# Performance work log

Hardware: AMD Instinct MI355X
Metric: run time of the kernel (lower is better)

The kernel has to match this reference:

```python
import jax, jax.numpy as jnp
import numpy as np

B, T, C, H, D = 2, 2048, 768, 12, 64
ATTN_MULT = 0.125  # 1/sqrt(head_dim)


def setup_inputs() -> dict:
    key = jax.random.key(0)
    k0, k1, k2 = jax.random.split(key, 3)
    x = jax.random.normal(k0, (B, T, C), jnp.float32)
    w_attn = jax.random.normal(k1, (3 * H * D, C), jnp.float32) * 0.02
    b_attn = jnp.zeros((3 * H * D,), jnp.float32)
    w_proj = jax.random.normal(k2, (C, H * D), jnp.float32) * 0.02
    b_proj = jnp.zeros((C,), jnp.float32)
    return {"x": x, "w_attn": w_attn, "b_attn": b_attn, "w_proj": w_proj, "b_proj": b_proj}


def reference(x, w_attn, b_attn, w_proj, b_proj):
    Bx, Tx, Cx = x.shape
    # fused qkv projection (torch nn.Linear: x @ W^T + b)
    qkv = x @ w_attn.T + b_attn                      # [B,T,3*H*D]
    q, k, v = jnp.split(qkv, 3, axis=2)
    def to_heads(t):
        return t.reshape(Bx, Tx, H, D).transpose(0, 2, 1, 3)  # [B,H,T,D]
    q, k, v = to_heads(q), to_heads(k), to_heads(v)
    att = jnp.einsum('bhqd,bhkd->bhqk', q, k) * ATTN_MULT     # [B,H,T,T]

    causal = jnp.tril(jnp.ones((Tx, Tx), dtype=bool))
    # selection scores from head 0 (selective attention)
    S = jax.nn.relu(att[:, 0])                                # [B,T,T]
    # prevent_from_masking_myself: zero diagonal; protect_bos_token: zero key col 0
    smask = causal & ~jnp.eye(Tx, dtype=bool)
    smask = smask.at[:, 0].set(False)
    S = jnp.where(smask, S, 0.0)
    # exclusive cumulative sum over the query dim: F[i,j] = sum_{i'<i} S[i',j]
    Fmask = jnp.cumsum(S, axis=-2) - S                        # [B,T,T]
    att = att - Fmask[:, None]                                # broadcast over heads

    att = jnp.where(causal, att, -jnp.inf)
    p = jax.nn.softmax(att, axis=-1)                          # [B,H,T,T]
    y = jnp.einsum('bhqk,bhkd->bhqd', p, v)                   # [B,H,T,D]
    y = y.transpose(0, 2, 1, 3).reshape(Bx, Tx, H * D)
    return y @ w_proj.T + b_proj
```

## Files before the change

kernel.cpp:

```cpp
#include <hip/hip_runtime.h>
#include <hip/hip_bf16.h>

#define BB 2
#define TT 2048
#define CC 768
#define HH 12
#define DD 64
#define NQKV 2304
#define MTOT (BB*TT)
#define CH 32
#define NCH (TT/CH)

typedef __bf16 bf16x8 __attribute__((ext_vector_type(8)));
typedef __bf16 bf16x4 __attribute__((ext_vector_type(4)));
typedef float  f32x4  __attribute__((ext_vector_type(4)));

__device__ __forceinline__ f32x4 mfma16(bf16x8 a, bf16x8 b, f32x4 c) {
    return __builtin_amdgcn_mfma_f32_16x16x32_bf16(a, b, c, 0, 0, 0);
}

__device__ __forceinline__ void load_lds16(const void* g, void* l) {
    __builtin_amdgcn_global_load_lds(
        (const __attribute__((address_space(1))) void*)g,
        (__attribute__((address_space(3))) void*)l, 16, 0, 0);
}

__global__ __launch_bounds__(256) void cvt_bf16_kernel(
    const float* __restrict__ x, const float* __restrict__ wa, const float* __restrict__ wp,
    __bf16* __restrict__ xb, __bf16* __restrict__ wab, __bf16* __restrict__ wpb)
{
    const long NX = (long)MTOT * CC;
    const long NWA = (long)NQKV * CC;
    long idx = ((long)blockIdx.x * 256 + threadIdx.x) * 4;
    const float* src; __bf16* dst; long off;
    if (idx < NX)            { src = x;  dst = xb;  off = idx; }
    else if (idx < NX + NWA) { src = wa; dst = wab; off = idx - NX; }
    else                     { src = wp; dst = wpb; off = idx - NX - NWA; }
    float4 v = *(const float4*)(src + off);
    bf16x4 o;
    o[0] = (__bf16)v.x; o[1] = (__bf16)v.y; o[2] = (__bf16)v.z; o[3] = (__bf16)v.w;
    *(bf16x4*)(dst + off) = o;
}

template<int EPI>
__global__ __launch_bounds__(256, 2) void gemm_nt_kernel(
    const __bf16* __restrict__ A, const __bf16* __restrict__ Bw,
    const float* __restrict__ bias,
    __bf16* __restrict__ oQ, __bf16* __restrict__ oK, __bf16* __restrict__ oVT,
    float* __restrict__ oOut, int K)
{
    __shared__ __align__(16) __bf16 As[128 * 32];
    __shared__ __align__(16) __bf16 Bs[128 * 32];
    const int tid = threadIdx.x;
    const int m0 = blockIdx.y * 128, n0 = blockIdx.x * 128;
    const int w = tid >> 6, lane = tid & 63, quad = lane >> 4, l16 = lane & 15;
    const int wm = (w >> 1) * 64, wn = (w & 1) * 64;
    const int grow = w * 16 + (lane >> 2);
    const int gcol = (lane & 3) * 8;
    __bf16* AsW = As + w * 512;
    __bf16* BsW = Bs + w * 512;

    f32x4 acc[4][4] = {};

    for (int kt = 0; kt < K; kt += 32) {
        __syncthreads();
        load_lds16(A  + (long)(m0 + grow) * K + kt + gcol,      AsW);
        load_lds16(A  + (long)(m0 + grow + 64) * K + kt + gcol, AsW + 2048);
        load_lds16(Bw + (long)(n0 + grow) * K + kt + gcol,      BsW);
        load_lds16(Bw + (long)(n0 + grow + 64) * K + kt + gcol, BsW + 2048);
        __syncthreads();

        bf16x8 af[4], bfr[4];
#pragma unroll
        for (int g = 0; g < 4; g++)  af[g]  = *(const bf16x8*)(As + (wm + g * 16 + l16) * 32 + quad * 8);
#pragma unroll
        for (int jb = 0; jb < 4; jb++) bfr[jb] = *(const bf16x8*)(Bs + (wn + jb * 16 + l16) * 32 + quad * 8);
#pragma unroll
        for (int g = 0; g < 4; g++)
#pragma unroll
            for (int jb = 0; jb < 4; jb++)
                acc[g][jb] = mfma16(af[g], bfr[jb], acc[g][jb]);
    }

#pragma unroll
    for (int jb = 0; jb < 4; jb++) {
        const int n = n0 + wn + jb * 16 + l16;
        const float bv = bias[n];
#pragma unroll
        for (int g = 0; g < 4; g++) {
#pragma unroll
            for (int r = 0; r < 4; r++) {
                const int m = m0 + wm + g * 16 + quad * 4 + r;
                const float v = acc[g][jb][r] + bv;
                if (EPI == 0) {
                    const int which = n / 768;
                    const int rem = n - which * 768;
                    const int h = rem >> 6, d = rem & 63;
                    const int b = m >> 11, t = m & 2047;
                    const __bf16 hv = (__bf16)v;
                    if (which == 0)      oQ [(((b * HH + h) * TT + t) << 6) + d] = hv;
                    else if (which == 1) oK [(((b * HH + h) * TT + t) << 6) + d] = hv;
                    else                 oVT[((((b * HH + h) << 6) + d) * TT) + t] = hv;
                } else {
                    oOut[(long)m * CC + n] = v;
                }
            }
        }
    }
}

__global__ __launch_bounds__(256) void sgemm_kernel(
    const __bf16* __restrict__ q, const __bf16* __restrict__ k, float* __restrict__ S)
{
    const int tj = blockIdx.x, ti = blockIdx.y, b = blockIdx.z;
    if (tj > ti) return;
    const int w = threadIdx.x >> 6, lane = threadIdx.x & 63, quad = lane >> 4, l16 = lane & 15;
    const int i0 = ti * 64 + w * 16;

    const __bf16* qp = q + (((long)(b * HH + 0) * TT + i0 + l16) << 6) + quad * 8;
    bf16x8 a0 = *(const bf16x8*)qp, a1 = *(const bf16x8*)(qp + 32);
    const __bf16* kbase = k + ((long)(b * HH + 0) * TT << 6);

#pragma unroll
    for (int jb = 0; jb < 4; jb++) {
        const __bf16* kp = kbase + (((long)(tj * 64 + jb * 16 + l16)) << 6) + quad * 8;
        bf16x8 b0 = *(const bf16x8*)kp, b1 = *(const bf16x8*)(kp + 32);
        f32x4 acc = {};
        acc = mfma16(a0, b0, acc);
        acc = mfma16(a1, b1, acc);
        const int j = tj * 64 + jb * 16 + l16;
#pragma unroll
        for (int r = 0; r < 4; r++) {
            const int i = i0 + quad * 4 + r;
            float v = fmaxf(acc[r] * 0.125f, 0.0f);
            v = (j >= 1 && j < i) ? v : 0.0f;
            S[((long)b * TT + i) * TT + j] = v;
        }
    }
}

__global__ __launch_bounds__(256) void scan_sum_kernel(
    const float* __restrict__ S, float* __restrict__ csum)
{
    const int j = blockIdx.x * 256 + threadIdx.x;
    const int chunk = blockIdx.y, b = blockIdx.z;
    const int ib = chunk * CH;
    const float* p = S + ((long)b * TT + ib) * TT + j;
    float s = 0.0f;
#pragma unroll
    for (int ii = 0; ii < CH; ii++) {
        float v = p[(long)ii * TT];
        s += ((ib + ii) > j) ? v : 0.0f;
    }
    csum[(b * NCH + chunk) * TT + j] = s;
}

__global__ __launch_bounds__(256) void scan_prefix_kernel(float* __restrict__ csum)
{
    const int idx = blockIdx.x * 256 + threadIdx.x;
    const int b = idx >> 11, j = idx & 2047;
    float vals[NCH];
#pragma unroll
    for (int c = 0; c < NCH; c++) vals[c] = csum[(b * NCH + c) * TT + j];
    float off = 0.0f;
#pragma unroll
    for (int c = 0; c < NCH; c++) { float t = vals[c]; vals[c] = off; off += t; }
#pragma unroll
    for (int c = 0; c < NCH; c++) csum[(b * NCH + c) * TT + j] = vals[c];
}

__global__ __launch_bounds__(256) void scan_write_kernel(
    float* __restrict__ S, const float* __restrict__ csum)
{
    const int j = blockIdx.x * 256 + threadIdx.x;
    const int chunk = blockIdx.y, b = blockIdx.z;
    const int ib = chunk * CH;
    float off = csum[(b * NCH + chunk) * TT + j];
    float* p = S + ((long)b * TT + ib) * TT + j;
#pragma unroll
    for (int ii = 0; ii < CH; ii++) {
        float v = p[(long)ii * TT];
        v = ((ib + ii) > j) ? v : 0.0f;
        p[(long)ii * TT] = off;
        off += v;
    }
}

__global__ __launch_bounds__(256, 3) void flash_kernel(
    const __bf16* __restrict__ q, const __bf16* __restrict__ k, const __bf16* __restrict__ vT,
    const float* __restrict__ F, __bf16* __restrict__ y)
{
    __shared__ __align__(16) __bf16 Ks[64 * 64];
    __shared__ __align__(16) __bf16 Vs[64 * 64];
    __shared__ __align__(16) __bf16 Pls[4][16 * 72];
    const int qt = 31 - blockIdx.x;
    const int h = blockIdx.y, b = blockIdx.z;
    const int w = threadIdx.x >> 6, lane = threadIdx.x & 63, quad = lane >> 4, l16 = lane & 15;
    const int i0 = qt * 64 + w * 16;

    const __bf16* qp = q + (((long)(b * HH + h) * TT + i0 + l16) << 6) + quad * 8;
    const bf16x8 aq0 = *(const bf16x8*)qp;
    const bf16x8 aq1 = *(const bf16x8*)(qp + 32);
    const __bf16* kb = k  + ((long)(b * HH + h) * TT << 6);
    const __bf16* vb = vT + ((long)(b * HH + h) * TT << 6);
    const float*  Fb = F  + (long)b * TT * TT + (long)i0 * TT;
    __bf16* Pl = &Pls[w][0];

    const int rl = lane >> 3;
    const int cs8 = ((lane & 7) ^ rl) * 8;
    __bf16* KsW = Ks + w * 1024;
    __bf16* VsW = Vs + w * 1024;
    const int sw0 = ((quad)     ^ (l16 & 7)) * 8;
    const int sw1 = ((quad + 4) ^ (l16 & 7)) * 8;

    f32x4 O[4] = {};
    float lr[4] = {0.0f, 0.0f, 0.0f, 0.0f};

    float Fn[4][4];
#pragma unroll
    for (int jh = 0; jh < 4; jh++)
#pragma unroll
        for (int r = 0; r < 4; r++)
            Fn[jh][r] = Fb[(long)(quad * 4 + r) * TT + jh * 16 + l16];

    const int jtend = qt * 64;
    for (int jt = 0; jt <= jtend; jt += 64) {
        __syncthreads();
        load_lds16(kb + ((long)(jt + w * 16 + rl) << 6) + cs8,     KsW);
        load_lds16(kb + ((long)(jt + w * 16 + 8 + rl) << 6) + cs8, KsW + 512);
        load_lds16(vb + (long)(w * 16 + rl) * TT + jt + cs8,       VsW);
        load_lds16(vb + (long)(w * 16 + 8 + rl) * TT + jt + cs8,   VsW + 512);
        float Fc[4][4];
#pragma unroll
        for (int jh = 0; jh < 4; jh++)
#pragma unroll
            for (int r = 0; r < 4; r++)
                Fc[jh][r] = Fn[jh][r];
        const int jn = (jt + 64 <= jtend) ? jt + 64 : jt;
#pragma unroll
        for (int jh = 0; jh < 4; jh++)
#pragma unroll
            for (int r = 0; r < 4; r++)
                Fn[jh][r] = Fb[(long)(quad * 4 + r) * TT + jn + jh * 16 + l16];
        __builtin_amdgcn_sched_barrier(0);
        __syncthreads();
        float sc[4][4];
#pragma unroll
        for (int jh = 0; jh < 4; jh++) {
            const bf16x8 kc0 = *(const bf16x8*)(Ks + ((jh * 16 + l16) << 6) + sw0);
            const bf16x8 kc1 = *(const bf16x8*)(Ks + ((jh * 16 + l16) << 6) + sw1);
            f32x4 acc = {};
            acc = mfma16(aq0, kc0, acc);
            acc = mfma16(aq1, kc1, acc);
#pragma unroll
            for (int r = 0; r < 4; r++) sc[jh][r] = acc[r];
        }
        const bool masked = (jt + 63 > i0);
#pragma unroll
        for (int jh = 0; jh < 4; jh++) {
            const int j = jt + jh * 16 + l16;
#pragma unroll
            for (int r = 0; r < 4; r++) {
                const int i = i0 + quad * 4 + r;
                float v = fmaf(sc[jh][r], 0.125f, -Fc[jh][r]);
                if (masked) v = (j <= i) ? v : -1e30f;
                const float p = __expf(fminf(v, 60.0f));
                sc[jh][r] = p;
                lr[r] += p;
            }
        }
#pragma unroll
        for (int r = 0; r < 4; r++) {
            const int il = quad * 4 + r;
#pragma unroll
            for (int jh = 0; jh < 4; jh++)
                Pl[il * 72 + jh * 16 + l16] = (__bf16)sc[jh][r];
        }
        const bf16x8 ap0 = *(const bf16x8*)(Pl + l16 * 72 + quad * 8);
        const bf16x8 ap1 = *(const bf16x8*)(Pl + l16 * 72 + 32 + quad * 8);
#pragma unroll
        for (int db = 0; db < 4; db++) {
            const bf16x8 vv0 = *(const bf16x8*)(Vs + ((db * 16 + l16) << 6) + sw0);
            const bf16x8 vv1 = *(const bf16x8*)(Vs + ((db * 16 + l16) << 6) + sw1);
            O[db] = mfma16(ap0, vv0, O[db]);
            O[db] = mfma16(ap1, vv1, O[db]);
        }
    }

    float inv[4];
#pragma unroll
    for (int r = 0; r < 4; r++) {
        float s = lr[r];
#pragma unroll
        for (int off = 8; off >= 1; off >>= 1) s += __shfl_xor(s, off, 16);
        inv[r] = 1.0f / s;
    }
#pragma unroll
    for (int db = 0; db < 4; db++) {
#pragma unroll
        for (int r = 0; r < 4; r++) {
            const int i = i0 + quad * 4 + r;
            y[((long)(b * TT + i)) * (HH * DD) + h * 64 + db * 16 + l16] = (__bf16)(O[db][r] * inv[r]);
        }
    }
}

extern "C" void kernel_launch(void* const* d_in, const int* in_sizes, int n_in,
                              void* d_out, int out_size, void* d_ws, size_t ws_size,
                              hipStream_t stream)
{
    const float* x      = (const float*)d_in[0];
    const float* w_attn = (const float*)d_in[1];
    const float* b_attn = (const float*)d_in[2];
    const float* w_proj = (const float*)d_in[3];
    const float* b_proj = (const float*)d_in[4];
    float* out = (float*)d_out;

    char* ws = (char*)d_ws;
    __bf16* xb  = (__bf16*)ws; ws += (long)MTOT * CC * 2;
    __bf16* wab = (__bf16*)ws; ws += (long)NQKV * CC * 2;
    __bf16* wpb = (__bf16*)ws; ws += (long)CC * (HH*DD) * 2;
    __bf16* qb  = (__bf16*)ws; ws += (long)BB * HH * TT * DD * 2;
    __bf16* kb  = (__bf16*)ws; ws += (long)BB * HH * TT * DD * 2;
    __bf16* vtb = (__bf16*)ws; ws += (long)BB * HH * TT * DD * 2;
    float*  SF  = (float*)ws;  ws += (long)BB * TT * TT * 4;
    float*  cs  = (float*)ws;  ws += (long)BB * NCH * TT * 4;
    __bf16* yb  = (__bf16*)ws; ws += (long)MTOT * (HH*DD) * 2;

    cvt_bf16_kernel<<<5376, 256, 0, stream>>>(x, w_attn, w_proj, xb, wab, wpb);
    gemm_nt_kernel<0><<<dim3(NQKV / 128, MTOT / 128), 256, 0, stream>>>(
        xb, wab, b_attn, qb, kb, vtb, nullptr, CC);
    sgemm_kernel<<<dim3(TT / 64, TT / 64, BB), 256, 0, stream>>>(qb, kb, SF);
    scan_sum_kernel<<<dim3(TT / 256, NCH, BB), 256, 0, stream>>>(SF, cs);
    scan_prefix_kernel<<<16, 256, 0, stream>>>(cs);
    scan_write_kernel<<<dim3(TT / 256, NCH, BB), 256, 0, stream>>>(SF, cs);
    flash_kernel<<<dim3(32, HH, BB), 256, 0, stream>>>(qb, kb, vtb, SF, yb);
    gemm_nt_kernel<1><<<dim3((HH*DD) / 128, MTOT / 128), 256, 0, stream>>>(
        yb, wpb, b_proj, nullptr, nullptr, nullptr, out, HH * DD);
}
```

Measured before the change: 228.0 us.

## Store selection scores and F mask in bf16; balance causal flash work per block

The S and cumulative F matrices are now stored in bf16 instead of fp32, and F is written to a separate buffer. This halves the memory traffic of the scan kernels and of the F reads inside the flash kernel. The flash kernel now runs 128-thread blocks, each handling two 32-row query tiles paired from opposite ends of the sequence to balance causal work. It also drops the F register prefetch and splits out an unmasked fast path for full tiles. bf16 storage of the large cumulative sums F loses precision, which may hurt accuracy.

```diff
diff --git a/kernel.cpp b/kernel.cpp
--- a/kernel.cpp
+++ b/kernel.cpp
@@ -110,7 +110,7 @@
 }
 
 __global__ __launch_bounds__(256) void sgemm_kernel(
-    const __bf16* __restrict__ q, const __bf16* __restrict__ k, float* __restrict__ S)
+    const __bf16* __restrict__ q, const __bf16* __restrict__ k, __bf16* __restrict__ S)
 {
     const int tj = blockIdx.x, ti = blockIdx.y, b = blockIdx.z;
     if (tj > ti) return;
@@ -134,22 +134,22 @@
             const int i = i0 + quad * 4 + r;
             float v = fmaxf(acc[r] * 0.125f, 0.0f);
             v = (j >= 1 && j < i) ? v : 0.0f;
-            S[((long)b * TT + i) * TT + j] = v;
+            S[((long)b * TT + i) * TT + j] = (__bf16)v;
         }
     }
 }
 
 __global__ __launch_bounds__(256) void scan_sum_kernel(
-    const float* __restrict__ S, float* __restrict__ csum)
+    const __bf16* __restrict__ S, float* __restrict__ csum)
 {
     const int j = blockIdx.x * 256 + threadIdx.x;
     const int chunk = blockIdx.y, b = blockIdx.z;
     const int ib = chunk * CH;
-    const float* p = S + ((long)b * TT + ib) * TT + j;
+    const __bf16* p = S + ((long)b * TT + ib) * TT + j;
     float s = 0.0f;
 #pragma unroll
     for (int ii = 0; ii < CH; ii++) {
-        float v = p[(long)ii * TT];
+        float v = (float)p[(long)ii * TT];
         s += ((ib + ii) > j) ? v : 0.0f;
     }
     csum[(b * NCH + chunk) * TT + j] = s;
@@ -170,137 +170,138 @@
 }
 
 __global__ __launch_bounds__(256) void scan_write_kernel(
-    float* __restrict__ S, const float* __restrict__ csum)
+    const __bf16* __restrict__ S, const float* __restrict__ csum, __bf16* __restrict__ Fo)
 {
     const int j = blockIdx.x * 256 + threadIdx.x;
     const int chunk = blockIdx.y, b = blockIdx.z;
     const int ib = chunk * CH;
     float off = csum[(b * NCH + chunk) * TT + j];
-    float* p = S + ((long)b * TT + ib) * TT + j;
+    const __bf16* ps = S  + ((long)b * TT + ib) * TT + j;
+    __bf16*       pf = Fo + ((long)b * TT + ib) * TT + j;
 #pragma unroll
     for (int ii = 0; ii < CH; ii++) {
-        float v = p[(long)ii * TT];
-        v = ((ib + ii) > j) ? v : 0.0f;
-        p[(long)ii * TT] = off;
+        float v = ((ib + ii) > j) ? (float)ps[(long)ii * TT] : 0.0f;
+        pf[(long)ii * TT] = (__bf16)off;
         off += v;
     }
 }
 
-__global__ __launch_bounds__(256, 3) void flash_kernel(
+__global__ __launch_bounds__(128, 2) void flash_kernel(
     const __bf16* __restrict__ q, const __bf16* __restrict__ k, const __bf16* __restrict__ vT,
-    const float* __restrict__ F, __bf16* __restrict__ y)
+    const __bf16* __restrict__ F, __bf16* __restrict__ y)
 {
     __shared__ __align__(16) __bf16 Ks[64 * 64];
     __shared__ __align__(16) __bf16 Vs[64 * 64];
-    __shared__ __align__(16) __bf16 Pls[4][16 * 72];
-    const int qt = 31 - blockIdx.x;
-    const int h = blockIdx.y, b = blockIdx.z;
+    __shared__ __align__(16) __bf16 Pls[2][16 * 72];
+    const int bid = blockIdx.x, h = blockIdx.y, b = blockIdx.z;
     const int w = threadIdx.x >> 6, lane = threadIdx.x & 63, quad = lane >> 4, l16 = lane & 15;
-    const int i0 = qt * 64 + w * 16;
-
-    const __bf16* qp = q + (((long)(b * HH + h) * TT + i0 + l16) << 6) + quad * 8;
-    const bf16x8 aq0 = *(const bf16x8*)qp;
-    const bf16x8 aq1 = *(const bf16x8*)(qp + 32);
+    const int rl = lane >> 3;
+    const int cs8 = ((lane & 7) ^ rl) * 8;
+    __bf16* KsW = Ks + w * 2048;
+    __bf16* VsW = Vs + w * 2048;
+    const int sw0 = ((quad)     ^ (l16 & 7)) * 8;
+    const int sw1 = ((quad + 4) ^ (l16 & 7)) * 8;
+    __bf16* Pl = &Pls[w][0];
     const __bf16* kb = k  + ((long)(b * HH + h) * TT << 6);
     const __bf16* vb = vT + ((long)(b * HH + h) * TT << 6);
-    const float*  Fb = F  + (long)b * TT * TT + (long)i0 * TT;
-    __bf16* Pl = &Pls[w][0];
-
-    const int rl = lane >> 3;
-    const int cs8 = ((lane & 7) ^ rl) * 8;
-    __bf16* KsW = Ks + w * 1024;
-    __bf16* VsW = Vs + w * 1024;
-    const int sw0 = ((quad)     ^ (l16 & 7)) * 8;
-    const int sw1 = ((quad + 4) ^ (l16 & 7)) * 8;
-
-    f32x4 O[4] = {};
-    float lr[4] = {0.0f, 0.0f, 0.0f, 0.0f};
-
-    float Fn[4][4];
-#pragma unroll
-    for (int jh = 0; jh < 4; jh++)
-#pragma unroll
-        for (int r = 0; r < 4; r++)
-            Fn[jh][r] = Fb[(long)(quad * 4 + r) * TT + jh * 16 + l16];
-
-    const int jtend = qt * 64;
-    for (int jt = 0; jt <= jtend; jt += 64) {
-        __syncthreads();
-        load_lds16(kb + ((long)(jt + w * 16 + rl) << 6) + cs8,     KsW);
-        load_lds16(kb + ((long)(jt + w * 16 + 8 + rl) << 6) + cs8, KsW + 512);
-        load_lds16(vb + (long)(w * 16 + rl) * TT + jt + cs8,       VsW);
-        load_lds16(vb + (long)(w * 16 + 8 + rl) * TT + jt + cs8,   VsW + 512);
-        float Fc[4][4];
-#pragma unroll
-        for (int jh = 0; jh < 4; jh++)
-#pragma unroll
-            for (int r = 0; r < 4; r++)
-                Fc[jh][r] = Fn[jh][r];
-        const int jn = (jt + 64 <= jtend) ? jt + 64 : jt;
-#pragma unroll
-        for (int jh = 0; jh < 4; jh++)
-#pragma unroll
-            for (int r = 0; r < 4; r++)
-                Fn[jh][r] = Fb[(long)(quad * 4 + r) * TT + jn + jh * 16 + l16];
-        __builtin_amdgcn_sched_barrier(0);
-        __syncthreads();
-        float sc[4][4];
-#pragma unroll
-        for (int jh = 0; jh < 4; jh++) {
-            const bf16x8 kc0 = *(const bf16x8*)(Ks + ((jh * 16 + l16) << 6) + sw0);
-            const bf16x8 kc1 = *(const bf16x8*)(Ks + ((jh * 16 + l16) << 6) + sw1);
-            f32x4 acc = {};
-            acc = mfma16(aq0, kc0, acc);
-            acc = mfma16(aq1, kc1, acc);
-#pragma unroll
-            for (int r = 0; r < 4; r++) sc[jh][r] = acc[r];
-        }
-        const bool masked = (jt + 63 > i0);
-#pragma unroll
-        for (int jh = 0; jh < 4; jh++) {
-            const int j = jt + jh * 16 + l16;
+
+    for (int ph = 0; ph < 2; ph++) {
+        const int qt = ph ? (63 - bid) : bid;
+        const int i0 = qt * 32 + w * 16;
+        const __bf16* qp = q + (((long)(b * HH + h) * TT + i0 + l16) << 6) + quad * 8;
+        const bf16x8 aq0 = *(const bf16x8*)qp;
+        const bf16x8 aq1 = *(const bf16x8*)(qp + 32);
+        const __bf16* Fb = F + (long)b * TT * TT + (long)i0 * TT;
+        f32x4 O[4] = {};
+        float lr[4] = {0.0f, 0.0f, 0.0f, 0.0f};
+        const int jtend = (qt >> 1) << 6;
+
+        for (int jt = 0; jt <= jtend; jt += 64) {
+            __syncthreads();
+#pragma unroll
+            for (int t = 0; t < 4; t++)
+                load_lds16(kb + ((long)(jt + w * 32 + t * 8 + rl) << 6) + cs8, KsW + t * 512);
+#pragma unroll
+            for (int t = 0; t < 4; t++)
+                load_lds16(vb + (long)(w * 32 + t * 8 + rl) * TT + jt + cs8, VsW + t * 512);
+            float Fc[4][4];
+#pragma unroll
+            for (int jh = 0; jh < 4; jh++)
+#pragma unroll
+                for (int r = 0; r < 4; r++)
+                    Fc[jh][r] = (float)Fb[(long)(quad * 4 + r) * TT + jt + jh * 16 + l16];
+            __syncthreads();
+            float sc[4][4];
+#pragma unroll
+            for (int jh = 0; jh < 4; jh++) {
+                const int jr = jh * 16 + l16;
+                const bf16x8 kc0 = *(const bf16x8*)(Ks + (jr << 6) + sw0);
+                const bf16x8 kc1 = *(const bf16x8*)(Ks + (jr << 6) + sw1);
+                f32x4 acc = {};
+                acc = mfma16(aq0, kc0, acc);
+                acc = mfma16(aq1, kc1, acc);
+#pragma unroll
+                for (int r = 0; r < 4; r++) sc[jh][r] = acc[r];
+            }
+            if (jt == jtend) {
+#pragma unroll
+                for (int jh = 0; jh < 4; jh++) {
+                    const int j = jt + jh * 16 + l16;
+#pragma unroll
+                    for (int r = 0; r < 4; r++) {
+                        const int i = i0 + quad * 4 + r;
+                        float v = fmaf(sc[jh][r], 0.125f, -Fc[jh][r]);
+                        v = (j <= i) ? v : -1e30f;
+                        const float p = __expf(fminf(v, 60.0f));
+                        sc[jh][r] = p;
+                        lr[r] += p;
+                    }
+                }
+            } else {
+#pragma unroll
+                for (int jh = 0; jh < 4; jh++) {
+#pragma unroll
+                    for (int r = 0; r < 4; r++) {
+                        float v = fmaf(sc[jh][r], 0.125f, -Fc[jh][r]);
+                        const float p = __expf(fminf(v, 60.0f));
+                        sc[jh][r] = p;
+                        lr[r] += p;
+                    }
+                }
+            }
+#pragma unroll
+            for (int r = 0; r < 4; r++) {
+                const int il = quad * 4 + r;
+#pragma unroll
+                for (int jh = 0; jh < 4; jh++)
+                    Pl[il * 72 + jh * 16 + l16] = (__bf16)sc[jh][r];
+            }
+            const bf16x8 ap0 = *(const bf16x8*)(Pl + l16 * 72 + quad * 8);
+            const bf16x8 ap1 = *(const bf16x8*)(Pl + l16 * 72 + 32 + quad * 8);
+#pragma unroll
+            for (int db = 0; db < 4; db++) {
+                const bf16x8 vv0 = *(const bf16x8*)(Vs + ((db * 16 + l16) << 6) + sw0);
+                const bf16x8 vv1 = *(const bf16x8*)(Vs + ((db * 16 + l16) << 6) + sw1);
+                O[db] = mfma16(ap0, vv0, O[db]);
+                O[db] = mfma16(ap1, vv1, O[db]);
+            }
+        }
+
+        float inv[4];
+#pragma unroll
+        for (int r = 0; r < 4; r++) {
+            float s = lr[r];
+#pragma unroll
+            for (int off = 8; off >= 1; off >>= 1) s += __shfl_xor(s, off, 16);
+            inv[r] = 1.0f / s;
+        }
+#pragma unroll
+        for (int db = 0; db < 4; db++) {
 #pragma unroll
             for (int r = 0; r < 4; r++) {
                 const int i = i0 + quad * 4 + r;
-                float v = fmaf(sc[jh][r], 0.125f, -Fc[jh][r]);
-                if (masked) v = (j <= i) ? v : -1e30f;
-                const float p = __expf(fminf(v, 60.0f));
-                sc[jh][r] = p;
-                lr[r] += p;
-            }
-        }
-#pragma unroll
-        for (int r = 0; r < 4; r++) {
-            const int il = quad * 4 + r;
-#pragma unroll
-            for (int jh = 0; jh < 4; jh++)
-                Pl[il * 72 + jh * 16 + l16] = (__bf16)sc[jh][r];
-        }
-        const bf16x8 ap0 = *(const bf16x8*)(Pl + l16 * 72 + quad * 8);
-        const bf16x8 ap1 = *(const bf16x8*)(Pl + l16 * 72 + 32 + quad * 8);
-#pragma unroll
-        for (int db = 0; db < 4; db++) {
-            const bf16x8 vv0 = *(const bf16x8*)(Vs + ((db * 16 + l16) << 6) + sw0);
-            const bf16x8 vv1 = *(const bf16x8*)(Vs + ((db * 16 + l16) << 6) + sw1);
-            O[db] = mfma16(ap0, vv0, O[db]);
-            O[db] = mfma16(ap1, vv1, O[db]);
-        }
-    }
-
-    float inv[4];
-#pragma unroll
-    for (int r = 0; r < 4; r++) {
-        float s = lr[r];
-#pragma unroll
-        for (int off = 8; off >= 1; off >>= 1) s += __shfl_xor(s, off, 16);
-        inv[r] = 1.0f / s;
-    }
-#pragma unroll
-    for (int db = 0; db < 4; db++) {
-#pragma unroll
-        for (int r = 0; r < 4; r++) {
-            const int i = i0 + quad * 4 + r;
-            y[((long)(b * TT + i)) * (HH * DD) + h * 64 + db * 16 + l16] = (__bf16)(O[db][r] * inv[r]);
+                y[((long)(b * TT + i)) * (HH * DD) + h * 64 + db * 16 + l16] = (__bf16)(O[db][r] * inv[r]);
+            }
         }
     }
 }
@@ -323,7 +324,8 @@
     __bf16* qb  = (__bf16*)ws; ws += (long)BB * HH * TT * DD * 2;
     __bf16* kb  = (__bf16*)ws; ws += (long)BB * HH * TT * DD * 2;
     __bf16* vtb = (__bf16*)ws; ws += (long)BB * HH * TT * DD * 2;
-    float*  SF  = (float*)ws;  ws += (long)BB * TT * TT * 4;
+    __bf16* SF  = (__bf16*)ws; ws += (long)BB * TT * TT * 2;
+    __bf16* Fo  = (__bf16*)ws; ws += (long)BB * TT * TT * 2;
     float*  cs  = (float*)ws;  ws += (long)BB * NCH * TT * 4;
     __bf16* yb  = (__bf16*)ws; ws += (long)MTOT * (HH*DD) * 2;
 
@@ -333,8 +335,8 @@
     sgemm_kernel<<<dim3(TT / 64, TT / 64, BB), 256, 0, stream>>>(qb, kb, SF);
     scan_sum_kernel<<<dim3(TT / 256, NCH, BB), 256, 0, stream>>>(SF, cs);
     scan_prefix_kernel<<<16, 256, 0, stream>>>(cs);
-    scan_write_kernel<<<dim3(TT / 256, NCH, BB), 256, 0, stream>>>(SF, cs);
-    flash_kernel<<<dim3(32, HH, BB), 256, 0, stream>>>(qb, kb, vtb, SF, yb);
+    scan_write_kernel<<<dim3(TT / 256, NCH, BB), 256, 0, stream>>>(SF, cs, Fo);
+    flash_kernel<<<dim3(32, HH, BB), 128, 0, stream>>>(qb, kb, vtb, Fo, yb);
     gemm_nt_kernel<1><<<dim3((HH*DD) / 128, MTOT / 128), 256, 0, stream>>>(
         yb, wpb, b_proj, nullptr, nullptr, nullptr, out, HH * DD);
 }
```

Result: faster. 220.1 us (-3.5%).
